# Kernel optimization log

Hardware: AMD Instinct MI355X
Metric: run time of the kernel (lower is better)

The kernel has to match this reference:

```python
import math
import jax, jax.numpy as jnp
import numpy as np

NUM_BUCKETS = 32
MAX_DISTANCE = 128
NUM_HEADS = 16


def _relative_position_bucket_bidirectional(relative_position):
    # encoder (is_decoder=False): split buckets for positive/negative, then log-spaced
    nb = NUM_BUCKETS // 2  # 16
    buckets = (relative_position > 0).astype(jnp.int32) * nb
    rp = jnp.abs(relative_position)
    max_exact = nb // 2  # 8
    is_small = rp < max_exact
    rp_safe = jnp.maximum(rp, 1)  # avoid log(0); masked out by is_small anyway
    large = max_exact + (
        jnp.log(rp_safe.astype(jnp.float32) / max_exact)
        / math.log(MAX_DISTANCE / max_exact)
        * (nb - max_exact)
    ).astype(jnp.int32)
    large = jnp.minimum(large, nb - 1)
    return buckets + jnp.where(is_small, rp, large)


def compute_bias(rel_bias, tgt_len, src_len):
    ctx = jnp.arange(tgt_len)[:, None]
    mem = jnp.arange(src_len)[None, :]
    buckets = _relative_position_bucket_bidirectional(mem - ctx)  # [T,S]
    values = rel_bias[buckets]            # [T,S,H]
    return jnp.transpose(values, (2, 0, 1))[None]  # [1,H,T,S]


def setup_inputs() -> dict:
    key = jax.random.key(0)
    ks = jax.random.split(key, 7)
    B, S, D = 4, 2048, 1024
    s = 1.0 / math.sqrt(D)
    return {
        "query_states": jax.random.normal(ks[0], (B, S, D), jnp.float32),
        "key_value_states": jax.random.normal(ks[1], (B, S, D), jnp.float32),
        "wq": jax.random.normal(ks[2], (D, D), jnp.float32) * s,
        "wk": jax.random.normal(ks[3], (D, D), jnp.float32) * s,
        "wv": jax.random.normal(ks[4], (D, D), jnp.float32) * s,
        "wo": jax.random.normal(ks[5], (D, D), jnp.float32) * s,
        "rel_bias": jax.random.normal(ks[6], (NUM_BUCKETS, NUM_HEADS), jnp.float32),
    }


def reference(query_states, key_value_states, wq, wk, wv, wo, rel_bias):
    B, T, D = query_states.shape
    S = key_value_states.shape[1]
    H = NUM_HEADS
    dh = D // H

    def shape(x, L):
        return jnp.transpose(x.reshape(B, L, H, dh), (0, 2, 1, 3))  # [B,H,L,dh]

    q = shape(query_states @ wq, T)
    k = shape(key_value_states @ wk, S)
    v = shape(key_value_states @ wv, S)

    bias = compute_bias(rel_bias, T, S)                      # [1,H,T,S]
    scores = jnp.einsum("bhtd,bhsd->bhts", q, k) + bias      # no 1/sqrt(d) scaling (T5)
    weights = jax.nn.softmax(scores, axis=-1)
    attn = jnp.einsum("bhts,bhsd->bhtd", weights, v)
    attn = jnp.transpose(attn, (0, 2, 1, 3)).reshape(B, T, D)
    return attn @ wo
```

## Files before the change

kernel.cpp:

```cpp
#include <hip/hip_runtime.h>
#include <hip/hip_bf16.h>
#include <math.h>

typedef __bf16 bf16;
typedef __attribute__((ext_vector_type(8))) __bf16 bf16x8;
typedef __attribute__((ext_vector_type(4))) __bf16 bf16x4;
typedef __attribute__((ext_vector_type(4))) float f32x4;
typedef __attribute__((ext_vector_type(16))) float f32x16;
typedef __attribute__((ext_vector_type(4), aligned(4))) float f32x4u;

#define B_  4
#define S_  2048
#define D_  1024
#define H_  16
#define DH_ 64
#define M_  (B_ * S_)
#define LOG2E 1.44269504088896f

static __device__ __forceinline__ f32x4 mfma16(bf16x8 a, bf16x8 b, f32x4 c) {
  return __builtin_amdgcn_mfma_f32_16x16x32_bf16(a, b, c, 0, 0, 0);
}
static __device__ __forceinline__ f32x16 mfma32(bf16x8 a, bf16x8 b, f32x16 c) {
  return __builtin_amdgcn_mfma_f32_32x32x16_bf16(a, b, c, 0, 0, 0);
}

static __device__ __forceinline__ void gld_lds16(const bf16* g, bf16* l) {
  __builtin_amdgcn_global_load_lds(
      (const __attribute__((address_space(1))) void*)g,
      (__attribute__((address_space(3))) void*)l, 16, 0, 0);
}

static __device__ __forceinline__ unsigned pkbf(float a, float b) {
  union { struct { __bf16 lo, hi; } s; unsigned u; } x;
  x.s.lo = (bf16)a; x.s.hi = (bf16)b;
  return x.u;
}

__global__ __launch_bounds__(256)
void cast2_kernel(const float* __restrict__ a, const float* __restrict__ bsrc,
                  bf16* __restrict__ oa, bf16* __restrict__ ob) {
  const int blk = blockIdx.x;
  const float* in = (blk < 8192) ? a : bsrc;
  bf16* out = (blk < 8192) ? oa : ob;
  size_t i = ((size_t)(blk & 8191) * 256 + threadIdx.x) * 4;
  float4 v = *(const float4*)(in + i);
  bf16x4 o = {(bf16)v.x, (bf16)v.y, (bf16)v.z, (bf16)v.w};
  *(bf16x4*)(out + i) = o;
}

__global__ __launch_bounds__(256)
void transpose_cast4_kernel(const float* __restrict__ w0, const float* __restrict__ w1,
                            const float* __restrict__ w2, const float* __restrict__ w3,
                            bf16* __restrict__ o0, bf16* __restrict__ o1,
                            bf16* __restrict__ o2, bf16* __restrict__ o3) {
  __shared__ float tile[32][33];
  const int z = blockIdx.z;
  const float* in = (z == 0) ? w0 : (z == 1) ? w1 : (z == 2) ? w2 : w3;
  bf16* out = (z == 0) ? o0 : (z == 1) ? o1 : (z == 2) ? o2 : o3;
  int n0 = blockIdx.x * 32, k0 = blockIdx.y * 32;
  int tx = threadIdx.x, ty = threadIdx.y;
#pragma unroll
  for (int j = 0; j < 32; j += 8)
    tile[ty + j][tx] = in[(size_t)(k0 + ty + j) * D_ + n0 + tx];
  __syncthreads();
#pragma unroll
  for (int j = 0; j < 32; j += 8)
    out[(size_t)(n0 + ty + j) * D_ + k0 + tx] = (bf16)tile[tx][ty + j];
}

__global__ __launch_bounds__(256)
void bias_table_kernel(const float* __restrict__ rel_bias, float* __restrict__ tab) {
  int i = blockIdx.x * 256 + threadIdx.x;
  int h = i >> 12, dp = i & 4095;
  int rel = dp - 2047;
  int bucket = (rel > 0) ? 16 : 0;
  int rp = rel < 0 ? -rel : rel;
  if (rp < 8) {
    bucket += rp;
  } else {
    int large = 8 + (int)(2.0f * __log2f((float)rp * 0.125f));
    bucket += (large < 15 ? large : 15);
  }
  tab[i] = rel_bias[bucket * H_ + h] * LOG2E - 64.0f;
}

__global__ __launch_bounds__(256)
void proj_gemm_kernel(const bf16* __restrict__ Xq, const bf16* __restrict__ Xkv,
                      const bf16* __restrict__ Wq, const bf16* __restrict__ Wk,
                      const bf16* __restrict__ Wv,
                      bf16* __restrict__ Qb, bf16* __restrict__ Kb, bf16* __restrict__ Vt) {
  const int K = D_;
  __shared__ bf16 As[128][64];
  __shared__ bf16 Bs[128][64];
  const int z = blockIdx.z;
  const bf16* A  = (z == 0) ? Xq : Xkv;
  const bf16* Bt = (z == 0) ? Wq : (z == 1) ? Wk : Wv;
  const int tid = threadIdx.x;
  const int brow = blockIdx.y * 128, bcol = blockIdx.x * 128;
  const int wave = tid >> 6, lane = tid & 63;
  const int wr = (wave >> 1) * 64, wc = (wave & 1) * 64;
  const int lrow = lane & 15, lgrp = lane >> 4;

  f32x4 acc[4][4] = {};

  const int srow8 = tid >> 3;
  const int scol = ((tid & 7) ^ (srow8 & 7)) * 8;
  const bf16* ag = A + (size_t)(brow + srow8) * K + scol;
  const bf16* bg = Bt + (size_t)(bcol + srow8) * K + scol;
  const size_t r32 = (size_t)32 * K;
  bf16* al = &As[0][0] + tid * 8;
  bf16* bl = &Bs[0][0] + tid * 8;

  const int rsw = (lrow & 7) << 4;
  const char* arp = (const char*)&As[0][0];
  const char* brp = (const char*)&Bs[0][0];

  for (int k0 = 0; k0 < K; k0 += 64) {
    __syncthreads();
    gld_lds16(ag + k0,           al);
    gld_lds16(ag + k0 + r32,     al + 2048);
    gld_lds16(ag + k0 + 2 * r32, al + 4096);
    gld_lds16(ag + k0 + 3 * r32, al + 6144);
    gld_lds16(bg + k0,           bl);
    gld_lds16(bg + k0 + r32,     bl + 2048);
    gld_lds16(bg + k0 + 2 * r32, bl + 4096);
    gld_lds16(bg + k0 + 3 * r32, bl + 6144);
    __syncthreads();
#pragma unroll
    for (int kk = 0; kk < 2; ++kk) {
      bf16x8 af[4], bfr[4];
#pragma unroll
      for (int i = 0; i < 4; ++i) {
        af[i]  = *(const bf16x8*)(arp + (wr + i * 16 + lrow) * 128 +
                                  ((kk * 64 + (lgrp << 4)) ^ rsw));
        bfr[i] = *(const bf16x8*)(brp + (wc + i * 16 + lrow) * 128 +
                                  ((kk * 64 + (lgrp << 4)) ^ rsw));
      }
#pragma unroll
      for (int mi = 0; mi < 4; ++mi)
#pragma unroll
        for (int ni = 0; ni < 4; ++ni)
          acc[mi][ni] = mfma16(af[mi], bfr[ni], acc[mi][ni]);
    }
  }

  const float scl = (z == 0) ? LOG2E : 1.0f;
#pragma unroll
  for (int mi = 0; mi < 4; ++mi) {
    const int rowb = brow + wr + mi * 16 + lgrp * 4;
#pragma unroll
    for (int ni = 0; ni < 4; ++ni) {
      const int col = bcol + wc + ni * 16 + lrow;
      const int hh = col >> 6, d = col & (DH_ - 1);
      if (z == 2) {
        const int bb = rowb >> 11, s = rowb & (S_ - 1);
        bf16x4 pk = {(bf16)acc[mi][ni][0], (bf16)acc[mi][ni][1],
                     (bf16)acc[mi][ni][2], (bf16)acc[mi][ni][3]};
        *(bf16x4*)&Vt[((size_t)((bb * H_ + hh) * DH_ + d)) * S_ + s] = pk;
      } else {
#pragma unroll
        for (int r = 0; r < 4; ++r) {
          const float v = acc[mi][ni][r] * scl;
          const int m = rowb + r;
          const int bb = m >> 11, s = m & (S_ - 1);
          if (z == 0)
            Qb[((size_t)((bb * H_ + hh) * S_ + s)) * DH_ + d] = (bf16)v;
          else
            Kb[((size_t)((bb * H_ + hh) * S_ + s)) * DH_ + d] = (bf16)v;
        }
      }
    }
  }
}

__global__ __launch_bounds__(256)
void gemm_out_kernel(const bf16* __restrict__ A, const bf16* __restrict__ Bt,
                     float* __restrict__ Cout) {
  const int K = D_, N = D_;
  __shared__ bf16 As[128][64];
  __shared__ bf16 Bs[128][64];
  const int tid = threadIdx.x;
  const int brow = blockIdx.y * 128, bcol = blockIdx.x * 128;
  const int wave = tid >> 6, lane = tid & 63;
  const int wr = (wave >> 1) * 64, wc = (wave & 1) * 64;
  const int lrow = lane & 15, lgrp = lane >> 4;

  f32x4 acc[4][4] = {};

  const int srow8 = tid >> 3;
  const int scol = ((tid & 7) ^ (srow8 & 7)) * 8;
  const bf16* ag = A + (size_t)(brow + srow8) * K + scol;
  const bf16* bg = Bt + (size_t)(bcol + srow8) * K + scol;
  const size_t r32 = (size_t)32 * K;
  bf16* al = &As[0][0] + tid * 8;
  bf16* bl = &Bs[0][0] + tid * 8;

  const int rsw = (lrow & 7) << 4;
  const char* arp = (const char*)&As[0][0];
  const char* brp = (const char*)&Bs[0][0];

  for (int k0 = 0; k0 < K; k0 += 64) {
    __syncthreads();
    gld_lds16(ag + k0,           al);
    gld_lds16(ag + k0 + r32,     al + 2048);
    gld_lds16(ag + k0 + 2 * r32, al + 4096);
    gld_lds16(ag + k0 + 3 * r32, al + 6144);
    gld_lds16(bg + k0,           bl);
    gld_lds16(bg + k0 + r32,     bl + 2048);
    gld_lds16(bg + k0 + 2 * r32, bl + 4096);
    gld_lds16(bg + k0 + 3 * r32, bl + 6144);
    __syncthreads();
#pragma unroll
    for (int kk = 0; kk < 2; ++kk) {
      bf16x8 af[4], bfr[4];
#pragma unroll
      for (int i = 0; i < 4; ++i) {
        af[i]  = *(const bf16x8*)(arp + (wr + i * 16 + lrow) * 128 +
                                  ((kk * 64 + (lgrp << 4)) ^ rsw));
        bfr[i] = *(const bf16x8*)(brp + (wc + i * 16 + lrow) * 128 +
                                  ((kk * 64 + (lgrp << 4)) ^ rsw));
      }
#pragma unroll
      for (int mi = 0; mi < 4; ++mi)
#pragma unroll
        for (int ni = 0; ni < 4; ++ni)
          acc[mi][ni] = mfma16(af[mi], bfr[ni], acc[mi][ni]);
    }
  }

#pragma unroll
  for (int mi = 0; mi < 4; ++mi) {
    const int rowb = brow + wr + mi * 16 + lgrp * 4;
#pragma unroll
    for (int ni = 0; ni < 4; ++ni) {
      const int col = bcol + wc + ni * 16 + lrow;
#pragma unroll
      for (int r = 0; r < 4; ++r)
        Cout[(size_t)(rowb + r) * N + col] = acc[mi][ni][r];
    }
  }
}

__global__ __launch_bounds__(256, 4)
void attn_kernel(const bf16* __restrict__ Q, const bf16* __restrict__ Kb,
                 const bf16* __restrict__ Vt, const float* __restrict__ tab,
                 bf16* __restrict__ Oa) {
  __shared__ bf16 SB[4][4096];

  const int bid = blockIdx.x;
  const int w = ((bid & 7) << 7) + (bid >> 3);
  const int qt = w & 15, h = (w >> 4) & 15, b = w >> 8;
  const int tid = threadIdx.x;
  const int wave = tid >> 6, lane = tid & 63;
  const int l31 = lane & 31;
  const int hi = lane >> 5;
  const int t = qt * 128 + wave * 32 + l31;

  const bf16* Qp = Q + (size_t)(b * H_ + h) * S_ * DH_;
  const bf16* Kp = Kb + (size_t)(b * H_ + h) * S_ * DH_;
  const bf16* Vp = Vt + (size_t)(b * H_ + h) * DH_ * S_;
  const float* btb = tab + h * 4096 + 2047 - t;

  const int row0 = tid >> 4, row1 = row0 + 16;
  const int colS = (tid & 15) << 4;
  const int col0 = colS ^ ((row0 & 15) << 4);
  const int col1 = colS ^ ((row1 & 15) << 4);
  const bf16* ks0 = Kp + (size_t)(row0 + 32 * (col0 >> 7)) * DH_ + ((col0 & 127) >> 1);
  const bf16* ks1 = Kp + (size_t)(row1 + 32 * (col1 >> 7)) * DH_ + ((col1 & 127) >> 1);
  const bf16* vs0 = Vp + (size_t)(row0 + 32 * (col0 >> 7)) * S_ + ((col0 & 127) >> 1);
  const bf16* vs1 = Vp + (size_t)(row1 + 32 * (col1 >> 7)) * S_ + ((col1 & 127) >> 1);
  bf16* sd = &SB[0][0] + tid * 8;

  const int swz = (l31 & 15) << 4;
  const char* rb = (const char*)&SB[0][0] + l31 * 256;
  const char* ra[4][2];
#pragma unroll
  for (int c = 0; c < 4; ++c)
#pragma unroll
    for (int sub = 0; sub < 2; ++sub)
      ra[c][sub] = rb + ((c * 32 + hi * 16 + sub * 128) ^ swz);

  bf16x8 qf[4];
#pragma unroll
  for (int c = 0; c < 4; ++c)
    qf[c] = *(const bf16x8*)&Qp[(size_t)t * DH_ + c * 16 + hi * 8];

  float l_r = 0.f;
  f32x16 o0 = {}, o1 = {};

  gld_lds16(ks0, sd); gld_lds16(ks1, sd + 2048);
  gld_lds16(vs0, sd + 8192); gld_lds16(vs1, sd + 10240);
  __syncthreads();

#define ATTN_TILE(BUF, S0)                                                        \
  {                                                                               \
    if ((S0) + 64 < S_) {                                                         \
      const int nb = (BUF) ^ 1;                                                   \
      gld_lds16(ks0 + (size_t)((S0) + 64) * DH_, sd + nb * 4096);                 \
      gld_lds16(ks1 + (size_t)((S0) + 64) * DH_, sd + nb * 4096 + 2048);          \
      gld_lds16(vs0 + ((S0) + 64), sd + nb * 4096 + 8192);                        \
      gld_lds16(vs1 + ((S0) + 64), sd + nb * 4096 + 10240);                       \
    }                                                                             \
    f32x16 sc0, sc1;                                                              \
    _Pragma("unroll")                                                             \
    for (int g = 0; g < 4; ++g) {                                                 \
      f32x4u b0 = *(const f32x4u*)(btb + (S0) + 8 * g + 4 * hi);                  \
      f32x4u b1 = *(const f32x4u*)(btb + (S0) + 32 + 8 * g + 4 * hi);             \
      _Pragma("unroll")                                                           \
      for (int v = 0; v < 4; ++v) { sc0[4 * g + v] = b0[v]; sc1[4 * g + v] = b1[v]; } \
    }                                                                             \
    _Pragma("unroll")                                                             \
    for (int c = 0; c < 4; ++c) {                                                 \
      bf16x8 k0 = *(const bf16x8*)(ra[c][0] + (BUF) * 8192);                      \
      bf16x8 k1 = *(const bf16x8*)(ra[c][1] + (BUF) * 8192);                      \
      sc0 = mfma32(k0, qf[c], sc0);                                               \
      sc1 = mfma32(k1, qf[c], sc1);                                               \
    }                                                                             \
    unsigned pw[16];                                                              \
    float q0s = 0.f, q1s = 0.f, q2s = 0.f, q3s = 0.f;                             \
    _Pragma("unroll")                                                             \
    for (int r2 = 0; r2 < 8; ++r2) {                                              \
      float a0 = __builtin_amdgcn_exp2f(sc0[2 * r2]);                             \
      float a1 = __builtin_amdgcn_exp2f(sc0[2 * r2 + 1]);                         \
      float c0 = __builtin_amdgcn_exp2f(sc1[2 * r2]);                             \
      float c1 = __builtin_amdgcn_exp2f(sc1[2 * r2 + 1]);                         \
      q0s += a0; q1s += a1; q2s += c0; q3s += c1;                                 \
      pw[r2] = pkbf(a0, a1);                                                      \
      pw[8 + r2] = pkbf(c0, c1);                                                  \
    }                                                                             \
    l_r += (q0s + q1s) + (q2s + q3s);                                             \
                 \
    unsigned sh[8];                                                               \
    _Pragma("unroll")                                                             \
    for (int g = 0; g < 4; ++g) {                                                 \
      const int base = (g & 1) * 4 + (g >> 1) * 8;                                \
      sh[2 * g]     = __shfl_xor(hi ? pw[base + 0] : pw[base + 2], 32);           \
      sh[2 * g + 1] = __shfl_xor(hi ? pw[base + 1] : pw[base + 3], 32);           \
    }                                                                             \
    _Pragma("unroll")                                                             \
    for (int g = 0; g < 4; ++g) {                                                 \
      const int base = (g & 1) * 4 + (g >> 1) * 8;                                \
      int4 bi = { (int)(hi ? sh[2 * g]     : pw[base + 0]),                       \
                  (int)(hi ? sh[2 * g + 1] : pw[base + 1]),                       \
                  (int)(hi ? pw[base + 2] : sh[2 * g]),                           \
                  (int)(hi ? pw[base + 3] : sh[2 * g + 1]) };                     \
      bf16x8 pb = *(bf16x8*)&bi;                                                  \
      bf16x8 v0 = *(const bf16x8*)(ra[g][0] + 16384 + (BUF) * 8192);              \
      bf16x8 v1 = *(const bf16x8*)(ra[g][1] + 16384 + (BUF) * 8192);              \
      o0 = mfma32(v0, pb, o0);                                                    \
      o1 = mfma32(v1, pb, o1);                                                    \
    }                                                                             \
    __syncthreads();                                                              \
  }

  for (int s0 = 0; s0 < S_; s0 += 128) {
    ATTN_TILE(0, s0)
    ATTN_TILE(1, s0 + 64)
  }
#undef ATTN_TILE

  l_r += __shfl_xor(l_r, 32);
  const float inv = 1.0f / l_r;
  bf16* Ob = Oa + ((size_t)(b * S_ + t)) * D_ + h * DH_;
#pragma unroll
  for (int g = 0; g < 4; ++g) {
    bf16x4 u0 = {(bf16)(o0[4 * g + 0] * inv), (bf16)(o0[4 * g + 1] * inv),
                 (bf16)(o0[4 * g + 2] * inv), (bf16)(o0[4 * g + 3] * inv)};
    *(bf16x4*)&Ob[8 * g + 4 * hi] = u0;
    bf16x4 u1 = {(bf16)(o1[4 * g + 0] * inv), (bf16)(o1[4 * g + 1] * inv),
                 (bf16)(o1[4 * g + 2] * inv), (bf16)(o1[4 * g + 3] * inv)};
    *(bf16x4*)&Ob[32 + 8 * g + 4 * hi] = u1;
  }
}

extern "C" void kernel_launch(void* const* d_in, const int* in_sizes, int n_in,
                              void* d_out, int out_size, void* d_ws, size_t ws_size,
                              hipStream_t stream) {
  const float* Xq   = (const float*)d_in[0];
  const float* Xkv  = (const float*)d_in[1];
  const float* Wq   = (const float*)d_in[2];
  const float* Wk   = (const float*)d_in[3];
  const float* Wv   = (const float*)d_in[4];
  const float* Wo   = (const float*)d_in[5];
  const float* relb = (const float*)d_in[6];
  float* out = (float*)d_out;

  char* ws = (char*)d_ws;
  const size_t SZ_X = (size_t)M_ * D_ * 2;
  const size_t SZ_W = (size_t)D_ * D_ * 2;
  bf16* Xq_b  = (bf16*)(ws);
  bf16* Xkv_b = (bf16*)(ws + SZ_X);
  bf16* Wq_t  = (bf16*)(ws + 2 * SZ_X);
  bf16* Wk_t  = (bf16*)(ws + 2 * SZ_X + SZ_W);
  bf16* Wv_t  = (bf16*)(ws + 2 * SZ_X + 2 * SZ_W);
  bf16* Wo_t  = (bf16*)(ws + 2 * SZ_X + 3 * SZ_W);
  bf16* Qb    = (bf16*)(ws + 2 * SZ_X + 4 * SZ_W);
  bf16* Kbuf  = (bf16*)(ws + 3 * SZ_X + 4 * SZ_W);
  bf16* Vt    = (bf16*)(ws + 4 * SZ_X + 4 * SZ_W);
  bf16* Ab    = (bf16*)(ws + 5 * SZ_X + 4 * SZ_W);
  float* tab  = (float*)(ws + 6 * SZ_X + 4 * SZ_W);

  cast2_kernel<<<16384, 256, 0, stream>>>(Xq, Xkv, Xq_b, Xkv_b);
  transpose_cast4_kernel<<<dim3(32, 32, 4), dim3(32, 8), 0, stream>>>(
      Wq, Wk, Wv, Wo, Wq_t, Wk_t, Wv_t, Wo_t);
  bias_table_kernel<<<256, 256, 0, stream>>>(relb, tab);

  proj_gemm_kernel<<<dim3(8, 64, 3), 256, 0, stream>>>(
      Xq_b, Xkv_b, Wq_t, Wk_t, Wv_t, Qb, Kbuf, Vt);
  attn_kernel<<<1024, 256, 0, stream>>>(Qb, Kbuf, Vt, tab, Ab);
  gemm_out_kernel<<<dim3(8, 64), 256, 0, stream>>>(Ab, Wo_t, out);
}
```

Before: 221.2 us.

## Remap GEMM blocks per XCD and double attention block query tile

Both GEMM kernels now use a 1-D grid and remap block IDs so that the blocks placed on each XCD cover a contiguous band of rows, which is meant to improve L2 reuse of the A and B tiles. The attention kernel grows to 512 threads (8 waves, 256 queries per block), so each staged K/V tile is shared by twice as many queries and each thread issues half as many global-to-LDS loads. Each block's shared-memory use stays the same, but the larger blocks halve the grid and raise register pressure under launch_bounds(512,4).

```diff
diff --git a/kernel.cpp b/kernel.cpp
--- a/kernel.cpp
+++ b/kernel.cpp
@@ -92,11 +92,15 @@
   const int K = D_;
   __shared__ bf16 As[128][64];
   __shared__ bf16 Bs[128][64];
-  const int z = blockIdx.z;
+  const int bid = blockIdx.x;
+  const int xcd = bid & 7, j = bid >> 3;
+  const int bx = j & 7;
+  const int p = (j >> 3) + xcd * 24;
+  const int by = p & 63, z = p >> 6;
   const bf16* A  = (z == 0) ? Xq : Xkv;
   const bf16* Bt = (z == 0) ? Wq : (z == 1) ? Wk : Wv;
   const int tid = threadIdx.x;
-  const int brow = blockIdx.y * 128, bcol = blockIdx.x * 128;
+  const int brow = by * 128, bcol = bx * 128;
   const int wave = tid >> 6, lane = tid & 63;
   const int wr = (wave >> 1) * 64, wc = (wave & 1) * 64;
   const int lrow = lane & 15, lgrp = lane >> 4;
@@ -179,8 +183,12 @@
   const int K = D_, N = D_;
   __shared__ bf16 As[128][64];
   __shared__ bf16 Bs[128][64];
+  const int bid = blockIdx.x;
+  const int xcd = bid & 7, j = bid >> 3;
+  const int bx = j & 7;
+  const int by = (j >> 3) + xcd * 8;
   const int tid = threadIdx.x;
-  const int brow = blockIdx.y * 128, bcol = blockIdx.x * 128;
+  const int brow = by * 128, bcol = bx * 128;
   const int wave = tid >> 6, lane = tid & 63;
   const int wr = (wave >> 1) * 64, wc = (wave & 1) * 64;
   const int lrow = lane & 15, lgrp = lane >> 4;
@@ -241,34 +249,31 @@
   }
 }
 
-__global__ __launch_bounds__(256, 4)
+__global__ __launch_bounds__(512, 4)
 void attn_kernel(const bf16* __restrict__ Q, const bf16* __restrict__ Kb,
                  const bf16* __restrict__ Vt, const float* __restrict__ tab,
                  bf16* __restrict__ Oa) {
   __shared__ bf16 SB[4][4096];
 
   const int bid = blockIdx.x;
-  const int w = ((bid & 7) << 7) + (bid >> 3);
-  const int qt = w & 15, h = (w >> 4) & 15, b = w >> 8;
+  const int w = ((bid & 7) << 6) + (bid >> 3);
+  const int qt = w & 7, h = (w >> 3) & 15, b = w >> 7;
   const int tid = threadIdx.x;
   const int wave = tid >> 6, lane = tid & 63;
   const int l31 = lane & 31;
   const int hi = lane >> 5;
-  const int t = qt * 128 + wave * 32 + l31;
+  const int t = qt * 256 + wave * 32 + l31;
 
   const bf16* Qp = Q + (size_t)(b * H_ + h) * S_ * DH_;
   const bf16* Kp = Kb + (size_t)(b * H_ + h) * S_ * DH_;
   const bf16* Vp = Vt + (size_t)(b * H_ + h) * DH_ * S_;
   const float* btb = tab + h * 4096 + 2047 - t;
 
-  const int row0 = tid >> 4, row1 = row0 + 16;
+  const int srow = tid >> 4;
   const int colS = (tid & 15) << 4;
-  const int col0 = colS ^ ((row0 & 15) << 4);
-  const int col1 = colS ^ ((row1 & 15) << 4);
-  const bf16* ks0 = Kp + (size_t)(row0 + 32 * (col0 >> 7)) * DH_ + ((col0 & 127) >> 1);
-  const bf16* ks1 = Kp + (size_t)(row1 + 32 * (col1 >> 7)) * DH_ + ((col1 & 127) >> 1);
-  const bf16* vs0 = Vp + (size_t)(row0 + 32 * (col0 >> 7)) * S_ + ((col0 & 127) >> 1);
-  const bf16* vs1 = Vp + (size_t)(row1 + 32 * (col1 >> 7)) * S_ + ((col1 & 127) >> 1);
+  const int scol = colS ^ ((srow & 15) << 4);
+  const bf16* ks0 = Kp + (size_t)(srow + 32 * (scol >> 7)) * DH_ + ((scol & 127) >> 1);
+  const bf16* vs0 = Vp + (size_t)(srow + 32 * (scol >> 7)) * S_ + ((scol & 127) >> 1);
   bf16* sd = &SB[0][0] + tid * 8;
 
   const int swz = (l31 & 15) << 4;
@@ -288,8 +293,8 @@
   float l_r = 0.f;
   f32x16 o0 = {}, o1 = {};
 
-  gld_lds16(ks0, sd); gld_lds16(ks1, sd + 2048);
-  gld_lds16(vs0, sd + 8192); gld_lds16(vs1, sd + 10240);
+  gld_lds16(ks0, sd);
+  gld_lds16(vs0, sd + 8192);
   __syncthreads();
 
 #define ATTN_TILE(BUF, S0)                                                        \
@@ -297,9 +302,7 @@
     if ((S0) + 64 < S_) {                                                         \
       const int nb = (BUF) ^ 1;                                                   \
       gld_lds16(ks0 + (size_t)((S0) + 64) * DH_, sd + nb * 4096);                 \
-      gld_lds16(ks1 + (size_t)((S0) + 64) * DH_, sd + nb * 4096 + 2048);          \
       gld_lds16(vs0 + ((S0) + 64), sd + nb * 4096 + 8192);                        \
-      gld_lds16(vs1 + ((S0) + 64), sd + nb * 4096 + 10240);                       \
     }                                                                             \
     f32x16 sc0, sc1;                                                              \
     _Pragma("unroll")                                                             \
@@ -405,8 +408,8 @@
       Wq, Wk, Wv, Wo, Wq_t, Wk_t, Wv_t, Wo_t);
   bias_table_kernel<<<256, 256, 0, stream>>>(relb, tab);
 
-  proj_gemm_kernel<<<dim3(8, 64, 3), 256, 0, stream>>>(
+  proj_gemm_kernel<<<1536, 256, 0, stream>>>(
       Xq_b, Xkv_b, Wq_t, Wk_t, Wv_t, Qb, Kbuf, Vt);
-  attn_kernel<<<1024, 256, 0, stream>>>(Qb, Kbuf, Vt, tab, Ab);
-  gemm_out_kernel<<<dim3(8, 64), 256, 0, stream>>>(Ab, Wo_t, out);
-}
+  attn_kernel<<<512, 512, 0, stream>>>(Qb, Kbuf, Vt, tab, Ab);
+  gemm_out_kernel<<<512, 256, 0, stream>>>(Ab, Wo_t, out);
+}
```

Measured after the change: 205.5 us (median of 2 runs). 7.1% less time.
